# Kernel optimization log

Hardware: AMD Instinct MI355X
Metric: run time of the kernel (lower is better)

The kernel has to match this reference:

```python
import jax, jax.numpy as jnp
import numpy as np

V = 50000
E = 640000
DIM = 128
NUM_EDGE_TYPES = 32


def setup_inputs() -> dict:
    key = jax.random.key(0)
    ks = jax.random.split(key, 8)
    return {
        "node_values": jax.random.normal(ks[0], (V, DIM), dtype=jnp.float32),
        "edge_src": jax.random.randint(ks[1], (E,), 0, V, dtype=jnp.int32),
        "edge_dest": jax.random.randint(ks[2], (E,), 0, V, dtype=jnp.int32),
        "edge_cls": jax.random.randint(ks[3], (E,), 0, NUM_EDGE_TYPES, dtype=jnp.int32),
        "W_src": jax.random.normal(ks[4], (DIM, DIM), dtype=jnp.float32) / np.sqrt(DIM),
        "b_src": jnp.zeros((DIM,), dtype=jnp.float32),
        "W_dest": jax.random.normal(ks[5], (DIM, DIM), dtype=jnp.float32) / np.sqrt(DIM),
        "b_dest": jnp.zeros((DIM,), dtype=jnp.float32),
        "edge_emb": jax.random.normal(ks[6], (NUM_EDGE_TYPES, DIM), dtype=jnp.float32),
    }


def reference(node_values, edge_src, edge_dest, edge_cls, W_src, b_src, W_dest, b_dest, edge_emb):
    # Dense projections over all nodes, then gather per edge (matches tf.gather(dense(...), idx))
    src_proj = node_values @ W_src + b_src    # [V, dim]
    dest_proj = node_values @ W_dest + b_dest  # [V, dim]
    # Per-edge fused message: gather src, gather dest, edge-class embedding lookup, add, relu
    msgs = jax.nn.relu(src_proj[edge_src] + dest_proj[edge_dest] + edge_emb[edge_cls])  # [E, dim]
    # Scatter-reduce messages onto destination nodes
    out = jax.ops.segment_sum(msgs, edge_dest, num_segments=V)  # [V, dim]
    return out
```

## Files before the change

### kernel.cpp

```cpp
#include <hip/hip_runtime.h>


#define V 50000
#define E 640000
#define DIM 128
#define NXCD 8
#define DRANGE 6250
#define NBIN_R 50
#define BINW 125
#define BINCAP 2048
#define NCHUNK 256
#define EC4 625
#define NE_MAX 512
#define QCAP 384

typedef __bf16 bf16x8 __attribute__((ext_vector_type(8)));
typedef float  f32x4  __attribute__((ext_vector_type(4)));
typedef float  f32x2  __attribute__((ext_vector_type(2)));

__device__ __forceinline__ float bf2f(unsigned int u16) {
    union { unsigned int i; float f; } c; c.i = u16 << 16; return c.f;
}
__device__ __forceinline__ unsigned int f2bf(float f) {
    union { float f; unsigned int i; } c; c.f = f;
    unsigned int u = c.i;
    return (u + 0x7FFFu + ((u >> 16) & 1u)) >> 16;
}

__global__ __launch_bounds__(256) void mp_binA(
    const int* __restrict__ ed, const int* __restrict__ es, const int* __restrict__ ec,
    const float* __restrict__ Ws, const float* __restrict__ Wd,
    const float* __restrict__ emb,
    unsigned short* __restrict__ Wpk, unsigned short* __restrict__ embB,
    int* __restrict__ binCnt, int* __restrict__ binbuf)
{
    __shared__ int ebuf[NE_MAX];
    __shared__ unsigned char bbin[NE_MAX];
    __shared__ int csr[NE_MAX];
    __shared__ unsigned char sbin[NE_MAX];
    __shared__ int hist[NBIN_R];
    __shared__ int lofs[NBIN_R + 1];
    __shared__ int lcur[NBIN_R];
    __shared__ int gbase[NBIN_R];
    __shared__ int ecnt;

    const int r = blockIdx.x & (NXCD - 1);
    const int c = blockIdx.x >> 3;
    const int dlo = r * DRANGE;
    const int t = threadIdx.x;

    if (blockIdx.x < 16) {
        int tid = blockIdx.x * 256 + t;
        int mat  = tid >> 11;
        int rem  = tid & 2047;
        int ct   = rem >> 8;
        int kt   = (rem >> 6) & 3;
        int lane = rem & 63;
        const float* W = mat ? Wd : Ws;
        int n  = ct * 16 + (lane & 15);
        int k0 = kt * 32 + (lane >> 4) * 8;
        unsigned short* dst = Wpk + (size_t)tid * 8;
        #pragma unroll
        for (int j = 0; j < 8; ++j) dst[j] = (unsigned short)f2bf(W[(k0 + j) * DIM + n]);
        embB[tid] = (unsigned short)f2bf(emb[tid]);
    }

    if (t < NBIN_R) hist[t] = 0;
    if (t == 0) ecnt = 0;
    __syncthreads();

    int4 DV[3], SV[3], CV[3];
    {
        const int4* ed4 = (const int4*)ed + c * EC4;
        const int4* es4 = (const int4*)es + c * EC4;
        const int4* ec4 = (const int4*)ec + c * EC4;
        #pragma unroll
        for (int k = 0; k < 3; ++k) {
            int i = t + k * 256;
            if (i < EC4) { DV[k] = ed4[i]; SV[k] = es4[i]; CV[k] = ec4[i]; }
            else { DV[k] = make_int4(-1, -1, -1, -1);
                   SV[k] = make_int4(0, 0, 0, 0); CV[k] = make_int4(0, 0, 0, 0); }
        }
    }

    #pragma unroll
    for (int k = 0; k < 3; ++k) {
        #define PUSH(D, S, C) { \
            int rel = (D) - dlo; \
            if ((unsigned)rel < DRANGE) { \
                int bin = (unsigned)rel / BINW; \
                int rl  = rel - bin * BINW; \
                atomicAdd(&hist[bin], 1); \
                int pos = atomicAdd(&ecnt, 1); \
                if (pos < NE_MAX) { \
                    ebuf[pos] = ((S) & 0xFFFF) | ((C) << 16) | (rl << 21); \
                    bbin[pos] = (unsigned char)bin; \
                } } }
        PUSH(DV[k].x, SV[k].x, CV[k].x); PUSH(DV[k].y, SV[k].y, CV[k].y);
        PUSH(DV[k].z, SV[k].z, CV[k].z); PUSH(DV[k].w, SV[k].w, CV[k].w);
        #undef PUSH
    }
    __syncthreads();

    if (t < NBIN_R) gbase[t] = atomicAdd(&binCnt[r * NBIN_R + t], hist[t]);
    if (t < 64) {
        int v = (t < NBIN_R) ? hist[t] : 0;
        #pragma unroll
        for (int dlt = 1; dlt < 64; dlt <<= 1) {
            int u = __shfl_up(v, dlt, 64);
            if (t >= dlt) v += u;
        }
        if (t < NBIN_R) { lofs[t + 1] = v; lcur[t] = v - hist[t]; }
        if (t == 0) lofs[0] = 0;
    }
    __syncthreads();

    int ne = ecnt; if (ne > NE_MAX) ne = NE_MAX;

    for (int i = t; i < ne; i += 256) {
        int b = bbin[i];
        int p = atomicAdd(&lcur[b], 1);
        csr[p] = ebuf[i];
        sbin[p] = (unsigned char)b;
    }
    __syncthreads();

    for (int i = t; i < ne; i += 256) {
        int b = sbin[i];
        int slot = gbase[b] + (i - lofs[b]);
        if (slot < BINCAP)
            binbuf[(r * NBIN_R + b) * BINCAP + slot] = csr[i];
    }
}

__global__ __launch_bounds__(256) void mp_proj(
    const float* __restrict__ x, const unsigned short* __restrict__ Wpk,
    const float* __restrict__ bs, const float* __restrict__ bd,
    unsigned char* __restrict__ ps8, unsigned short* __restrict__ pdB)
{
    __shared__ float stage[4][16 * 132];
    const int wave = __builtin_amdgcn_readfirstlane(threadIdx.x) >> 6;
    const int lane = threadIdx.x & 63;
    const int m = lane & 15, q = lane >> 4;
    const int row0 = blockIdx.x * 64 + wave * 16;

    int arow = row0 + m; if (arow >= V) arow = V - 1;
    const float* xr = x + (size_t)arow * DIM + q * 8;

    bf16x8 A[4];
    #pragma unroll
    for (int kt = 0; kt < 4; ++kt) {
        float4 u = *(const float4*)(xr + kt * 32);
        float4 v = *(const float4*)(xr + kt * 32 + 4);
        bf16x8 a;
        a[0] = (__bf16)u.x; a[1] = (__bf16)u.y; a[2] = (__bf16)u.z; a[3] = (__bf16)u.w;
        a[4] = (__bf16)v.x; a[5] = (__bf16)v.y; a[6] = (__bf16)v.z; a[7] = (__bf16)v.w;
        A[kt] = a;
    }

    const bf16x8* Bp = (const bf16x8*)Wpk;

    f32x4 accS[8], accD[8];
    #pragma unroll
    for (int ct = 0; ct < 8; ++ct) {
        f32x4 aS = {0.f, 0.f, 0.f, 0.f}, aD = {0.f, 0.f, 0.f, 0.f};
        #pragma unroll
        for (int kt = 0; kt < 4; ++kt) {
            bf16x8 bS = Bp[((0 * 8 + ct) * 4 + kt) * 64 + lane];
            bf16x8 bD = Bp[((1 * 8 + ct) * 4 + kt) * 64 + lane];
            aS = __builtin_amdgcn_mfma_f32_16x16x32_bf16(A[kt], bS, aS, 0, 0, 0);
            aD = __builtin_amdgcn_mfma_f32_16x16x32_bf16(A[kt], bD, aD, 0, 0, 0);
        }
        accS[ct] = aS; accD[ct] = aD;
    }

    float* st = stage[wave];
    const int rr = lane & 15, cg = lane >> 4;
    const int orow = row0 + rr;
    const float* rowp = st + rr * 132 + cg * 32;

    #pragma unroll
    for (int ct = 0; ct < 8; ++ct) {
        const float bv = bs[ct * 16 + m];
        #pragma unroll
        for (int r = 0; r < 4; ++r)
            st[(q * 4 + r) * 132 + ct * 16 + m] = accS[ct][r] + bv;
    }
    __syncthreads();
    {
        int w[8];
        #pragma unroll
        for (int j = 0; j < 8; ++j) {
            float4 f = *(const float4*)(rowp + 4 * j);
            int v = __builtin_amdgcn_cvt_pk_fp8_f32(f.x, f.y, 0, false);
            v = __builtin_amdgcn_cvt_pk_fp8_f32(f.z, f.w, v, true);
            w[j] = v;
        }
        if (orow < V) {
            int4* dst = (int4*)(ps8 + (size_t)orow * 128 + cg * 32);
            dst[0] = make_int4(w[0], w[1], w[2], w[3]);
            dst[1] = make_int4(w[4], w[5], w[6], w[7]);
        }
    }
    __syncthreads();

    #pragma unroll
    for (int ct = 0; ct < 8; ++ct) {
        const float bv = bd[ct * 16 + m];
        #pragma unroll
        for (int r = 0; r < 4; ++r)
            st[(q * 4 + r) * 132 + ct * 16 + m] = accD[ct][r] + bv;
    }
    __syncthreads();
    {
        int w[16];
        #pragma unroll
        for (int j = 0; j < 8; ++j) {
            float4 f = *(const float4*)(rowp + 4 * j);
            w[2 * j]     = f2bf(f.x) | (f2bf(f.y) << 16);
            w[2 * j + 1] = f2bf(f.z) | (f2bf(f.w) << 16);
        }
        if (orow < V) {
            int4* dst = (int4*)(pdB + (size_t)orow * 128 + cg * 32);
            #pragma unroll
            for (int jj = 0; jj < 4; ++jj)
                dst[jj] = make_int4(w[4 * jj], w[4 * jj + 1], w[4 * jj + 2], w[4 * jj + 3]);
        }
    }
}

__global__ __launch_bounds__(256) void mp_binBC(
    const unsigned char* __restrict__ ps8, const unsigned short* __restrict__ pdB,
    const unsigned short* __restrict__ embB,
    const int* __restrict__ binCnt, const int* __restrict__ binbuf,
    float* __restrict__ out)
{
    __shared__ int csr[QCAP];
    __shared__ int cnt[16];
    __shared__ int off[17];
    __shared__ int cur[16];

    const int r = blockIdx.x & (NXCD - 1);
    const int rest = blockIdx.x >> 3;
    const int bi = rest % NBIN_R;
    const int qu = rest / NBIN_R;
    const int bin = r * NBIN_R + bi;
    const int rel0 = qu * 16;
    const int relW = (qu == 7) ? 13 : 16;
    const int d0 = bin * BINW + rel0;
    const int t = threadIdx.x;
    const int wave = t >> 6, lane = t & 63;

    int nb = binCnt[bin]; if (nb > BINCAP) nb = BINCAP;
    const int* buf = binbuf + (size_t)bin * BINCAP;

    if (t < 16) cnt[t] = 0;

    int EB[8];
    #pragma unroll
    for (int k = 0; k < 8; ++k) {
        int i = t + k * 256;
        EB[k] = (i < nb) ? buf[i] : -1;
    }

    float dp0v[4], dp1v[4];
    #pragma unroll
    for (int k = 0; k < 4; ++k) {
        int rl = wave + k * 4;
        int d = d0 + ((rl < relW) ? rl : 0);
        unsigned int pdu = *(const unsigned int*)(pdB + (size_t)d * DIM + 2 * lane);
        dp0v[k] = bf2f(pdu & 0xFFFF); dp1v[k] = bf2f(pdu >> 16);
    }
    __syncthreads();

    #pragma unroll
    for (int k = 0; k < 8; ++k) {
        int rl = (int)((unsigned)EB[k] >> 21) - rel0;
        if ((unsigned)rl < (unsigned)relW) atomicAdd(&cnt[rl], 1);
    }
    __syncthreads();

    if (t < 16) {
        int v = (t < relW) ? cnt[t] : 0;
        #pragma unroll
        for (int dlt = 1; dlt < 16; dlt <<= 1) {
            int u = __shfl_up(v, dlt, 64);
            if (t >= dlt) v += u;
        }
        off[t + 1] = v;
        cur[t] = v - cnt[t];
        if (t == 0) off[0] = 0;
    }
    __syncthreads();

    #pragma unroll
    for (int k = 0; k < 8; ++k) {
        int rl = (int)((unsigned)EB[k] >> 21) - rel0;
        if ((unsigned)rl < (unsigned)relW) {
            int pos = atomicAdd(&cur[rl], 1);
            if (pos < QCAP) csr[pos] = EB[k];
        }
    }
    __syncthreads();

    #define PROC(P) { \
        int s_ = *(const unsigned short*)(ps8 + ((size_t)((P) & 0xFFFF) << 7) + 2 * lane); \
        unsigned int e_ = *(const unsigned int*)(embB + ((((P) >> 16) & 0x1F) << 7) + 2 * lane); \
        f32x2 f_ = __builtin_amdgcn_cvt_pk_f32_fp8(s_, false); \
        a0 += fmaxf(f_.x + dp0 + bf2f(e_ & 0xFFFF), 0.f); \
        a1 += fmaxf(f_.y + dp1 + bf2f(e_ >> 16),    0.f); }

    #pragma unroll
    for (int k = 0; k < 4; ++k) {
        const int rl = wave + k * 4;
        if (rl >= relW) break;
        const int d = d0 + rl;
        int i0 = off[rl], i1 = off[rl + 1];
        if (i1 > QCAP) i1 = QCAP;
        if (i0 > i1) i0 = i1;
        const float dp0 = dp0v[k], dp1 = dp1v[k];
        float a0 = 0.f, a1 = 0.f;
        int i = i0;
        for (; i + 8 <= i1; i += 8) {
            int p0 = csr[i],     p1 = csr[i + 1], p2 = csr[i + 2], p3 = csr[i + 3];
            int p4 = csr[i + 4], p5 = csr[i + 5], p6 = csr[i + 6], p7 = csr[i + 7];
            PROC(p0); PROC(p1); PROC(p2); PROC(p3);
            PROC(p4); PROC(p5); PROC(p6); PROC(p7);
        }
        for (; i + 4 <= i1; i += 4) {
            int p0 = csr[i], p1 = csr[i + 1], p2 = csr[i + 2], p3 = csr[i + 3];
            PROC(p0); PROC(p1); PROC(p2); PROC(p3);
        }
        for (; i < i1; ++i) { int p0 = csr[i]; PROC(p0); }
        *(float2*)(out + (size_t)d * DIM + 2 * lane) = make_float2(a0, a1);
    }
    #undef PROC
}

extern "C" void kernel_launch(void* const* d_in, const int* in_sizes, int n_in,
                              void* d_out, int out_size, void* d_ws, size_t ws_size,
                              hipStream_t stream) {
    const float* x   = (const float*)d_in[0];
    const int*   es  = (const int*)d_in[1];
    const int*   ed  = (const int*)d_in[2];
    const int*   ec  = (const int*)d_in[3];
    const float* Ws  = (const float*)d_in[4];
    const float* bs  = (const float*)d_in[5];
    const float* Wd  = (const float*)d_in[6];
    const float* bd  = (const float*)d_in[7];
    const float* emb = (const float*)d_in[8];
    float* out = (float*)d_out;

    char* ws = (char*)d_ws;
    size_t off = 0;
    unsigned char*  ps8  = (unsigned char*)(ws + off);  off += (size_t)V * 128;
    unsigned short* pdB  = (unsigned short*)(ws + off); off += (size_t)V * DIM * 2;
    int* binbuf = (int*)(ws + off);                     off += (size_t)400 * BINCAP * 4;
    int* binCnt = (int*)(ws + off);                     off += 400 * 4;
    unsigned short* Wpk  = (unsigned short*)(ws + off); off += 2 * 128 * 128 * 2;
    unsigned short* embB = (unsigned short*)(ws + off); off += 32 * 128 * 2;

    hipMemsetAsync(binCnt, 0, 400 * 4, stream);
    mp_binA<<<NXCD * NCHUNK, 256, 0, stream>>>(ed, es, ec, Ws, Wd, emb, Wpk, embB, binCnt, binbuf);
    mp_proj<<<(V + 63) / 64, 256, 0, stream>>>(x, Wpk, bs, bd, ps8, pdB);
    mp_binBC<<<NBIN_R * NXCD * 8, 256, 0, stream>>>(ps8, pdB, embB, binCnt, binbuf, out);
}
```

Measured before the change: 154.3 us.

## Fuse edge binning and node projection into one interleaved-role kernel

Moves the weight/embedding packing and the binCnt zeroing into a small setup kernel that replaces the memset. The edge binning and the MFMA node projection now run in one launch: block roles are interleaved two binning blocks to one projection block, so the memory-bound binning overlaps the compute-heavy projection and a launch gap disappears. In exchange every block reserves the combined LDS of both roles, which can lower occupancy, and the kernel count does not drop because the setup kernel is added.

```diff
diff --git a/kernel.cpp b/kernel.cpp
--- a/kernel.cpp
+++ b/kernel.cpp
@@ -13,6 +13,7 @@
 #define EC4 625
 #define NE_MAX 512
 #define QCAP 384
+#define NPROJ 782
 
 typedef __bf16 bf16x8 __attribute__((ext_vector_type(8)));
 typedef float  f32x4  __attribute__((ext_vector_type(4)));
@@ -27,12 +28,34 @@
     return (u + 0x7FFFu + ((u >> 16) & 1u)) >> 16;
 }
 
-__global__ __launch_bounds__(256) void mp_binA(
-    const int* __restrict__ ed, const int* __restrict__ es, const int* __restrict__ ec,
+__global__ __launch_bounds__(256) void mp_setup(
     const float* __restrict__ Ws, const float* __restrict__ Wd,
     const float* __restrict__ emb,
     unsigned short* __restrict__ Wpk, unsigned short* __restrict__ embB,
-    int* __restrict__ binCnt, int* __restrict__ binbuf)
+    int* __restrict__ binCnt)
+{
+    int tid = blockIdx.x * 256 + threadIdx.x;
+    int mat  = tid >> 11;
+    int rem  = tid & 2047;
+    int ct   = rem >> 8;
+    int kt   = (rem >> 6) & 3;
+    int lane = rem & 63;
+    const float* W = mat ? Wd : Ws;
+    int n  = ct * 16 + (lane & 15);
+    int k0 = kt * 32 + (lane >> 4) * 8;
+    unsigned short* dst = Wpk + (size_t)tid * 8;
+    #pragma unroll
+    for (int j = 0; j < 8; ++j) dst[j] = (unsigned short)f2bf(W[(k0 + j) * DIM + n]);
+    embB[tid] = (unsigned short)f2bf(emb[tid]);
+    if (tid < NXCD * NBIN_R) binCnt[tid] = 0;
+}
+
+__global__ __launch_bounds__(256) void mp_fused(
+    const int* __restrict__ ed, const int* __restrict__ es, const int* __restrict__ ec,
+    int* __restrict__ binCnt, int* __restrict__ binbuf,
+    const float* __restrict__ x, const unsigned short* __restrict__ Wpk,
+    const float* __restrict__ bs, const float* __restrict__ bd,
+    unsigned char* __restrict__ ps8, unsigned short* __restrict__ pdB)
 {
     __shared__ int ebuf[NE_MAX];
     __shared__ unsigned char bbin[NE_MAX];
@@ -43,106 +66,93 @@
     __shared__ int lcur[NBIN_R];
     __shared__ int gbase[NBIN_R];
     __shared__ int ecnt;
-
-    const int r = blockIdx.x & (NXCD - 1);
-    const int c = blockIdx.x >> 3;
-    const int dlo = r * DRANGE;
+    __shared__ float stage[4][16 * 132];
+
+    const int b = blockIdx.x;
+    const int role = b % 3;
     const int t = threadIdx.x;
 
-    if (blockIdx.x < 16) {
-        int tid = blockIdx.x * 256 + t;
-        int mat  = tid >> 11;
-        int rem  = tid & 2047;
-        int ct   = rem >> 8;
-        int kt   = (rem >> 6) & 3;
-        int lane = rem & 63;
-        const float* W = mat ? Wd : Ws;
-        int n  = ct * 16 + (lane & 15);
-        int k0 = kt * 32 + (lane >> 4) * 8;
-        unsigned short* dst = Wpk + (size_t)tid * 8;
-        #pragma unroll
-        for (int j = 0; j < 8; ++j) dst[j] = (unsigned short)f2bf(W[(k0 + j) * DIM + n]);
-        embB[tid] = (unsigned short)f2bf(emb[tid]);
-    }
-
-    if (t < NBIN_R) hist[t] = 0;
-    if (t == 0) ecnt = 0;
-    __syncthreads();
-
-    int4 DV[3], SV[3], CV[3];
-    {
-        const int4* ed4 = (const int4*)ed + c * EC4;
-        const int4* es4 = (const int4*)es + c * EC4;
-        const int4* ec4 = (const int4*)ec + c * EC4;
+    if (role != 2) {
+        const int chunk = (b / 3) * 2 + role;
+        const int r = chunk & (NXCD - 1);
+        const int c = chunk >> 3;
+        const int dlo = r * DRANGE;
+
+        if (t < NBIN_R) hist[t] = 0;
+        if (t == 0) ecnt = 0;
+        __syncthreads();
+
+        int4 DV[3], SV[3], CV[3];
+        {
+            const int4* ed4 = (const int4*)ed + c * EC4;
+            const int4* es4 = (const int4*)es + c * EC4;
+            const int4* ec4 = (const int4*)ec + c * EC4;
+            #pragma unroll
+            for (int k = 0; k < 3; ++k) {
+                int i = t + k * 256;
+                if (i < EC4) { DV[k] = ed4[i]; SV[k] = es4[i]; CV[k] = ec4[i]; }
+                else { DV[k] = make_int4(-1, -1, -1, -1);
+                       SV[k] = make_int4(0, 0, 0, 0); CV[k] = make_int4(0, 0, 0, 0); }
+            }
+        }
+
         #pragma unroll
         for (int k = 0; k < 3; ++k) {
-            int i = t + k * 256;
-            if (i < EC4) { DV[k] = ed4[i]; SV[k] = es4[i]; CV[k] = ec4[i]; }
-            else { DV[k] = make_int4(-1, -1, -1, -1);
-                   SV[k] = make_int4(0, 0, 0, 0); CV[k] = make_int4(0, 0, 0, 0); }
-        }
-    }
-
-    #pragma unroll
-    for (int k = 0; k < 3; ++k) {
-        #define PUSH(D, S, C) { \
-            int rel = (D) - dlo; \
-            if ((unsigned)rel < DRANGE) { \
-                int bin = (unsigned)rel / BINW; \
-                int rl  = rel - bin * BINW; \
-                atomicAdd(&hist[bin], 1); \
-                int pos = atomicAdd(&ecnt, 1); \
-                if (pos < NE_MAX) { \
-                    ebuf[pos] = ((S) & 0xFFFF) | ((C) << 16) | (rl << 21); \
-                    bbin[pos] = (unsigned char)bin; \
-                } } }
-        PUSH(DV[k].x, SV[k].x, CV[k].x); PUSH(DV[k].y, SV[k].y, CV[k].y);
-        PUSH(DV[k].z, SV[k].z, CV[k].z); PUSH(DV[k].w, SV[k].w, CV[k].w);
-        #undef PUSH
-    }
-    __syncthreads();
-
-    if (t < NBIN_R) gbase[t] = atomicAdd(&binCnt[r * NBIN_R + t], hist[t]);
-    if (t < 64) {
-        int v = (t < NBIN_R) ? hist[t] : 0;
-        #pragma unroll
-        for (int dlt = 1; dlt < 64; dlt <<= 1) {
-            int u = __shfl_up(v, dlt, 64);
-            if (t >= dlt) v += u;
-        }
-        if (t < NBIN_R) { lofs[t + 1] = v; lcur[t] = v - hist[t]; }
-        if (t == 0) lofs[0] = 0;
-    }
-    __syncthreads();
-
-    int ne = ecnt; if (ne > NE_MAX) ne = NE_MAX;
-
-    for (int i = t; i < ne; i += 256) {
-        int b = bbin[i];
-        int p = atomicAdd(&lcur[b], 1);
-        csr[p] = ebuf[i];
-        sbin[p] = (unsigned char)b;
-    }
-    __syncthreads();
-
-    for (int i = t; i < ne; i += 256) {
-        int b = sbin[i];
-        int slot = gbase[b] + (i - lofs[b]);
-        if (slot < BINCAP)
-            binbuf[(r * NBIN_R + b) * BINCAP + slot] = csr[i];
-    }
-}
-
-__global__ __launch_bounds__(256) void mp_proj(
-    const float* __restrict__ x, const unsigned short* __restrict__ Wpk,
-    const float* __restrict__ bs, const float* __restrict__ bd,
-    unsigned char* __restrict__ ps8, unsigned short* __restrict__ pdB)
-{
-    __shared__ float stage[4][16 * 132];
+            #define PUSH(D, S, C) { \
+                int rel = (D) - dlo; \
+                if ((unsigned)rel < DRANGE) { \
+                    int bin = (unsigned)rel / BINW; \
+                    int rl  = rel - bin * BINW; \
+                    atomicAdd(&hist[bin], 1); \
+                    int pos = atomicAdd(&ecnt, 1); \
+                    if (pos < NE_MAX) { \
+                        ebuf[pos] = ((S) & 0xFFFF) | ((C) << 16) | (rl << 21); \
+                        bbin[pos] = (unsigned char)bin; \
+                    } } }
+            PUSH(DV[k].x, SV[k].x, CV[k].x); PUSH(DV[k].y, SV[k].y, CV[k].y);
+            PUSH(DV[k].z, SV[k].z, CV[k].z); PUSH(DV[k].w, SV[k].w, CV[k].w);
+            #undef PUSH
+        }
+        __syncthreads();
+
+        if (t < NBIN_R) gbase[t] = atomicAdd(&binCnt[r * NBIN_R + t], hist[t]);
+        if (t < 64) {
+            int v = (t < NBIN_R) ? hist[t] : 0;
+            #pragma unroll
+            for (int dlt = 1; dlt < 64; dlt <<= 1) {
+                int u = __shfl_up(v, dlt, 64);
+                if (t >= dlt) v += u;
+            }
+            if (t < NBIN_R) { lofs[t + 1] = v; lcur[t] = v - hist[t]; }
+            if (t == 0) lofs[0] = 0;
+        }
+        __syncthreads();
+
+        int ne = ecnt; if (ne > NE_MAX) ne = NE_MAX;
+
+        for (int i = t; i < ne; i += 256) {
+            int bb = bbin[i];
+            int p = atomicAdd(&lcur[bb], 1);
+            csr[p] = ebuf[i];
+            sbin[p] = (unsigned char)bb;
+        }
+        __syncthreads();
+
+        for (int i = t; i < ne; i += 256) {
+            int bb = sbin[i];
+            int slot = gbase[bb] + (i - lofs[bb]);
+            if (slot < BINCAP)
+                binbuf[(r * NBIN_R + bb) * BINCAP + slot] = csr[i];
+        }
+        return;
+    }
+
+    const int p = b / 3;
+    if (p >= NPROJ) return;
     const int wave = __builtin_amdgcn_readfirstlane(threadIdx.x) >> 6;
     const int lane = threadIdx.x & 63;
     const int m = lane & 15, q = lane >> 4;
-    const int row0 = blockIdx.x * 64 + wave * 16;
+    const int row0 = p * 64 + wave * 16;
 
     int arow = row0 + m; if (arow >= V) arow = V - 1;
     const float* xr = x + (size_t)arow * DIM + q * 8;
@@ -183,8 +193,8 @@
     for (int ct = 0; ct < 8; ++ct) {
         const float bv = bs[ct * 16 + m];
         #pragma unroll
-        for (int r = 0; r < 4; ++r)
-            st[(q * 4 + r) * 132 + ct * 16 + m] = accS[ct][r] + bv;
+        for (int rg = 0; rg < 4; ++rg)
+            st[(q * 4 + rg) * 132 + ct * 16 + m] = accS[ct][rg] + bv;
     }
     __syncthreads();
     {
@@ -208,8 +218,8 @@
     for (int ct = 0; ct < 8; ++ct) {
         const float bv = bd[ct * 16 + m];
         #pragma unroll
-        for (int r = 0; r < 4; ++r)
-            st[(q * 4 + r) * 132 + ct * 16 + m] = accD[ct][r] + bv;
+        for (int rg = 0; rg < 4; ++rg)
+            st[(q * 4 + rg) * 132 + ct * 16 + m] = accD[ct][rg] + bv;
     }
     __syncthreads();
     {
@@ -360,8 +370,8 @@
     unsigned short* Wpk  = (unsigned short*)(ws + off); off += 2 * 128 * 128 * 2;
     unsigned short* embB = (unsigned short*)(ws + off); off += 32 * 128 * 2;
 
-    hipMemsetAsync(binCnt, 0, 400 * 4, stream);
-    mp_binA<<<NXCD * NCHUNK, 256, 0, stream>>>(ed, es, ec, Ws, Wd, emb, Wpk, embB, binCnt, binbuf);
-    mp_proj<<<(V + 63) / 64, 256, 0, stream>>>(x, Wpk, bs, bd, ps8, pdB);
+    mp_setup<<<16, 256, 0, stream>>>(Ws, Wd, emb, Wpk, embB, binCnt);
+    mp_fused<<<3072, 256, 0, stream>>>(ed, es, ec, binCnt, binbuf,
+                                       x, Wpk, bs, bd, ps8, pdB);
     mp_binBC<<<NBIN_R * NXCD * 8, 256, 0, stream>>>(ps8, pdB, embB, binCnt, binbuf, out);
 }
```

Result: faster. 145.0 us (-6.0%).
